# Kernel tuning notes

Hardware: AMD Instinct MI355X
Metric: run time of the kernel (lower is better)

Reference implementation:

```python
import jax, jax.numpy as jnp
import numpy as np

N = 8192
PT_DIM = 3
ENC_DIM = 384
RADIUS = 0.12
ALPHA = 6.0
SQRT_D = ENC_DIM ** 0.5


def setup_inputs() -> dict:
    key = jax.random.key(0)
    k1, k2 = jax.random.split(key)
    pts = jax.random.uniform(k1, (N, PT_DIM), dtype=jnp.float32)  # points in unit cube
    # A corresponds to the (frozen) random-feature matrix: stacked standard normals * alpha
    A = jax.random.normal(k2, (PT_DIM, ENC_DIM), dtype=jnp.float32) * ALPHA
    return {"pts": pts, "A": A}


def reference(pts, A):
    # Radius-ball adjacency: J[i,j] = 1 if ||pts[i]-pts[j]|| < r (dist^2 < r^2, dist >= 0)
    d2 = jnp.sum((pts[:, None, :] - pts[None, :, :]) ** 2, axis=-1)  # (N, N)
    J = (d2 < RADIUS * RADIUS).astype(pts.dtype)                      # (N, N)

    pA = (pts / RADIUS) @ A            # (N, ENC_DIM)
    c, s = jnp.cos(pA), jnp.sin(pA)    # epA = [cos(pA), sin(pA)]

    # Neighbor aggregation: G = J @ epA, done per real/imag part
    Gr = J @ c                          # (N, ENC_DIM)
    Gi = J @ s

    # Complex phase division: (Gr + i Gi) / (cos + i sin)
    G = jax.lax.complex(Gr, Gi) / jax.lax.complex(c, s)

    # Row-wise normalization to norm sqrt(enc_dim)
    G = G / jnp.linalg.norm(G, axis=-1, keepdims=True) * SQRT_D
    return G
```

## Files before the change

### kernel.cpp

```cpp
#include <hip/hip_runtime.h>
#include <hip/hip_fp16.h>
#include <math.h>

#define N_PTS   8192
#define ENC     384
#define NTHREAD 384
#define MAXNB   512
#define NCELL1  8
#define NCELLS  512
#define RADIUS  0.12f

__device__ __forceinline__ void fast_sincos(float x, float& s, float& c) {
    float rev = x * 0.15915494309189535f;
    rev -= rintf(rev);
    s = __builtin_amdgcn_sinf(rev);
    c = __builtin_amdgcn_cosf(rev);
}

__device__ __forceinline__ int cell_of(float x) {
    int c = (int)(x * 8.0f);
    return min(NCELL1 - 1, max(0, c));
}

static const size_t OFF_START_I  = 0;
static const size_t OFF_CURSOR_I = 520;
static const size_t OFF_CELLID_I = 1032;
static const size_t OFF_ORIG_I   = 9224;
static const size_t INT_REGION_B = 17416u * 4;
static const size_t OFF_SPTS_B   = INT_REGION_B;
static const size_t OFF_CS_B     = OFF_SPTS_B + 131072;
static const size_t WS_FULL_B    = OFF_CS_B + (size_t)(N_PTS + 1) * ENC * 2 * 2;
static const size_t WS_SMALL_B   = OFF_CS_B;

__global__ __launch_bounds__(1024) void k_count_scan(const float* __restrict__ pts,
                                                     int* __restrict__ cell_id,
                                                     int* __restrict__ cell_start,
                                                     int* __restrict__ cursor) {
    __shared__ int cnt[NCELLS];
    __shared__ int sc[NCELLS];
    const int t = threadIdx.x;
    if (t < NCELLS) cnt[t] = 0;
    __syncthreads();
    for (int i = t; i < N_PTS; i += 1024) {
        int cx = cell_of(pts[3 * i + 0]);
        int cy = cell_of(pts[3 * i + 1]);
        int cz = cell_of(pts[3 * i + 2]);
        int c = (cx * NCELL1 + cy) * NCELL1 + cz;
        cell_id[i] = c;
        atomicAdd(&cnt[c], 1);
    }
    __syncthreads();
    if (t < NCELLS) sc[t] = cnt[t];
    __syncthreads();
    for (int off = 1; off < NCELLS; off <<= 1) {
        int v = 0;
        if (t < NCELLS && t >= off) v = sc[t - off];
        __syncthreads();
        if (t < NCELLS) sc[t] += v;
        __syncthreads();
    }
    if (t < NCELLS) {
        int excl = sc[t] - cnt[t];
        cell_start[t] = excl;
        cursor[t] = excl;
    }
    if (t == 0) cell_start[NCELLS] = N_PTS;
}

__global__ __launch_bounds__(256) void k_scatter(const float* __restrict__ pts,
                                                 const int* __restrict__ cell_id,
                                                 int* __restrict__ cursor,
                                                 int* __restrict__ orig,
                                                 float4* __restrict__ spts) {
    int i = blockIdx.x * 256 + threadIdx.x;
    if (i >= N_PTS) return;
    int c = cell_id[i];
    int pos = atomicAdd(&cursor[c], 1);
    orig[pos] = i;
    spts[pos] = make_float4(pts[3 * i + 0], pts[3 * i + 1], pts[3 * i + 2], 0.f);
}

__global__ __launch_bounds__(NTHREAD) void k_encode(const float4* __restrict__ spts,
                                                    const float* __restrict__ A,
                                                    __half2* __restrict__ cs) {
    const int p = blockIdx.x;
    const int t = threadIdx.x;
    if (p == N_PTS) {
        cs[(size_t)p * ENC + t] = __floats2half2_rn(0.f, 0.f);
        return;
    }
    float4 P = spts[p];
    float qx = __fdiv_rn(P.x, RADIUS);
    float qy = __fdiv_rn(P.y, RADIUS);
    float qz = __fdiv_rn(P.z, RADIUS);
    float a0 = A[t], a1 = A[ENC + t], a2 = A[2 * ENC + t];
    float pa = fmaf(qz, a2, fmaf(qy, a1, qx * a0));
    float s, c;
    fast_sincos(pa, s, c);
    cs[(size_t)p * ENC + t] = __floats2half2_rn(c, s);
}

__global__ __launch_bounds__(NTHREAD) void k_main(const float4* __restrict__ spts,
                                                  const int* __restrict__ orig,
                                                  const int* __restrict__ cell_start,
                                                  const uint4* __restrict__ cs4,
                                                  const float* __restrict__ A,
                                                  float* __restrict__ out, int out_mode) {
    const int p = (blockIdx.x % 8) * (N_PTS / 8) + blockIdx.x / 8;
    const int t = threadIdx.x, lane = t & 63, wid = t >> 6;

    __shared__ unsigned short nb_idx[MAXNB];
    __shared__ int   nb_cnt;
    __shared__ float comb_a[96][8];
    __shared__ float comb_b[96][8];
    __shared__ float red2[96];
    __shared__ float red_tot;
    if (t == 0) nb_cnt = 0;
    __syncthreads();

    const float4 Pi = spts[p];
    const float xi = Pi.x, yi = Pi.y, zi = Pi.z;
    const double dxi = (double)xi, dyi = (double)yi, dzi = (double)zi;
    const double R2 = (double)0.12 * (double)0.12;
    const float R2_LO = 0.0144f - 1e-6f;
    const float R2_HI = 0.0144f + 1e-6f;

    const int cx = cell_of(xi), cy = cell_of(yi), cz = cell_of(zi);
    const int zlo = max(cz - 1, 0), zhi = min(cz + 1, NCELL1 - 1);

    for (int r = wid; r < 9; r += NTHREAD / 64) {
        int cxx = cx + (r / 3) - 1;
        int cyy = cy + (r % 3) - 1;
        if (cxx < 0 || cxx >= NCELL1 || cyy < 0 || cyy >= NCELL1) continue;
        int base_c = (cxx * NCELL1 + cyy) * NCELL1;
        int lo = cell_start[base_c + zlo];
        int hi = cell_start[base_c + zhi + 1];
        for (int jb = lo; jb < hi; jb += 64) {
            int j = jb + lane;
            bool isnb = false;
            if (j < hi) {
                float4 Pj = spts[j];
                float fdx = Pj.x - xi, fdy = Pj.y - yi, fdz = Pj.z - zi;
                float d2f = fmaf(fdx, fdx, fmaf(fdy, fdy, fdz * fdz));
                if (d2f < R2_LO) {
                    isnb = true;
                } else if (d2f <= R2_HI) {
                    double ddx = (double)Pj.x - dxi, ddy = (double)Pj.y - dyi, ddz = (double)Pj.z - dzi;
                    isnb = (ddx * ddx + ddy * ddy + ddz * ddz) < R2;
                }
            }
            unsigned long long mask = __ballot(isnb);
            if (mask) {
                int leader = __ffsll((long long)mask) - 1;
                int basep = 0;
                if (lane == leader) basep = atomicAdd(&nb_cnt, __popcll(mask));
                basep = __shfl(basep, leader);
                if (isnb) {
                    int pos = basep + __popcll(mask & ((1ull << lane) - 1ull));
                    if (pos < MAXNB) nb_idx[pos] = (unsigned short)j;
                }
            }
        }
    }
    __syncthreads();
    const int nn = min(nb_cnt, MAXNB);
    if (t < 4) {
        int idx = nn + t;
        if (idx < MAXNB) nb_idx[idx] = (unsigned short)N_PTS;
    }
    __syncthreads();
    const int nn_pad = (nn + 3) & ~3;

    const int g = t / 96, q = t - g * 96;
    float4 accR = make_float4(0.f, 0.f, 0.f, 0.f);
    float4 accI = make_float4(0.f, 0.f, 0.f, 0.f);

    #pragma unroll 4
    for (int m = 0; m < nn_pad; m += 4) {
        int j = min((int)nb_idx[m + g], N_PTS);
        uint4 u = cs4[j * 96 + q];
        float2 f0 = __half22float2(*reinterpret_cast<__half2*>(&u.x));
        float2 f1 = __half22float2(*reinterpret_cast<__half2*>(&u.y));
        float2 f2 = __half22float2(*reinterpret_cast<__half2*>(&u.z));
        float2 f3 = __half22float2(*reinterpret_cast<__half2*>(&u.w));
        accR.x += f0.x; accI.x += f0.y;
        accR.y += f1.x; accI.y += f1.y;
        accR.z += f2.x; accI.z += f2.y;
        accR.w += f3.x; accI.w += f3.y;
    }

    if (g == 1) {
        float* d = comb_a[q];
        d[0]=accR.x; d[1]=accR.y; d[2]=accR.z; d[3]=accR.w;
        d[4]=accI.x; d[5]=accI.y; d[6]=accI.z; d[7]=accI.w;
    } else if (g == 3) {
        float* d = comb_b[q];
        d[0]=accR.x; d[1]=accR.y; d[2]=accR.z; d[3]=accR.w;
        d[4]=accI.x; d[5]=accI.y; d[6]=accI.z; d[7]=accI.w;
    }
    __syncthreads();
    if (g == 0) {
        const float* s = comb_a[q];
        accR.x+=s[0]; accR.y+=s[1]; accR.z+=s[2]; accR.w+=s[3];
        accI.x+=s[4]; accI.y+=s[5]; accI.z+=s[6]; accI.w+=s[7];
    } else if (g == 2) {
        const float* s = comb_b[q];
        accR.x+=s[0]; accR.y+=s[1]; accR.z+=s[2]; accR.w+=s[3];
        accI.x+=s[4]; accI.y+=s[5]; accI.z+=s[6]; accI.w+=s[7];
    }
    __syncthreads();
    if (g == 2) {
        float* d = comb_a[q];
        d[0]=accR.x; d[1]=accR.y; d[2]=accR.z; d[3]=accR.w;
        d[4]=accI.x; d[5]=accI.y; d[6]=accI.z; d[7]=accI.w;
    }
    __syncthreads();
    if (g == 0) {
        const float* s = comb_a[q];
        accR.x+=s[0]; accR.y+=s[1]; accR.z+=s[2]; accR.w+=s[3];
        accI.x+=s[4]; accI.y+=s[5]; accI.z+=s[6]; accI.w+=s[7];
    }

    if (g == 0) {
        float m2 = accR.x*accR.x + accI.x*accI.x + accR.y*accR.y + accI.y*accI.y
                 + accR.z*accR.z + accI.z*accI.z + accR.w*accR.w + accI.w*accI.w;
        red2[q] = m2;
    }
    __syncthreads();
    if (t < 64) {
        float v = red2[t] + (t < 32 ? red2[64 + t] : 0.f);
        #pragma unroll
        for (int off = 32; off > 0; off >>= 1) v += __shfl_down(v, off);
        if (t == 0) red_tot = v;
    }
    __syncthreads();

    if (g == 0) {
        const float scale = sqrtf(384.0f / red_tot);
        const float qx = __fdiv_rn(xi, RADIUS);
        const float qy = __fdiv_rn(yi, RADIUS);
        const float qz = __fdiv_rn(zi, RADIUS);
        const int d0 = 4 * q;
        float re[4], im[4];
        #pragma unroll
        for (int k = 0; k < 4; ++k) {
            int d = d0 + k;
            float pa = fmaf(qz, A[2 * ENC + d], fmaf(qy, A[ENC + d], qx * A[d]));
            float sv, cv;
            fast_sincos(pa, sv, cv);
            float gr = (k==0)?accR.x:(k==1)?accR.y:(k==2)?accR.z:accR.w;
            float gi = (k==0)?accI.x:(k==1)?accI.y:(k==2)?accI.z:accI.w;
            re[k] = (gr * cv + gi * sv) * scale;
            im[k] = (gi * cv - gr * sv) * scale;
        }
        const int o = orig[p];
        if (out_mode == 0) {
            ((float4*)out)[o * 96 + q] = make_float4(re[0], re[1], re[2], re[3]);
        } else {
            ((float4*)out)[o * 192 + 2 * q + 0] = make_float4(re[0], im[0], re[1], im[1]);
            ((float4*)out)[o * 192 + 2 * q + 1] = make_float4(re[2], im[2], re[3], im[3]);
        }
    }
}

__global__ __launch_bounds__(NTHREAD) void vecKM_allpairs(const float* __restrict__ pts,
                                                          const float* __restrict__ A,
                                                          float* __restrict__ out, int out_mode) {
    const int i = blockIdx.x;
    const int t = threadIdx.x;
    __shared__ float nb_x[MAXNB], nb_y[MAXNB], nb_z[MAXNB];
    __shared__ int nb_cnt;
    __shared__ float red[8];
    if (t == 0) nb_cnt = 0;
    __syncthreads();
    const float xi = pts[3 * i + 0], yi = pts[3 * i + 1], zi = pts[3 * i + 2];
    const double dxi = xi, dyi = yi, dzi = zi;
    const double R2 = (double)0.12 * (double)0.12;
    const float R2_LO = 0.0144f - 1e-6f, R2_HI = 0.0144f + 1e-6f;
    const int lane = t & 63;
    for (int jb = 0; jb < N_PTS; jb += NTHREAD) {
        const int j = jb + t;
        bool isnb = false;
        float xj = 0.f, yj = 0.f, zj = 0.f;
        if (j < N_PTS) {
            xj = pts[3 * j + 0]; yj = pts[3 * j + 1]; zj = pts[3 * j + 2];
            float fdx = xj - xi, fdy = yj - yi, fdz = zj - zi;
            float d2f = fmaf(fdx, fdx, fmaf(fdy, fdy, fdz * fdz));
            if (d2f < R2_LO) isnb = true;
            else if (d2f <= R2_HI) {
                double dx = (double)xj - dxi, dy = (double)yj - dyi, dz = (double)zj - dzi;
                isnb = (dx * dx + dy * dy + dz * dz) < R2;
            }
        }
        unsigned long long mask = __ballot(isnb);
        if (mask) {
            int leader = __ffsll((long long)mask) - 1;
            int basep = 0;
            if (lane == leader) basep = atomicAdd(&nb_cnt, __popcll(mask));
            basep = __shfl(basep, leader);
            if (isnb) {
                int pos = basep + __popcll(mask & ((1ull << lane) - 1ull));
                if (pos < MAXNB) {
                    nb_x[pos] = (xj - xi) * (1.0f / 0.12f);
                    nb_y[pos] = (yj - yi) * (1.0f / 0.12f);
                    nb_z[pos] = (zj - zi) * (1.0f / 0.12f);
                }
            }
        }
    }
    __syncthreads();
    const int nn = min(nb_cnt, MAXNB);
    const float a0 = A[t], a1 = A[ENC + t], a2 = A[2 * ENC + t];
    float gr = 0.f, gi = 0.f;
    #pragma unroll 4
    for (int m = 0; m < nn; ++m) {
        float pa = fmaf(nb_z[m], a2, fmaf(nb_y[m], a1, nb_x[m] * a0));
        float sv, cv;
        fast_sincos(pa, sv, cv);
        gr += cv; gi += sv;
    }
    float m2 = fmaf(gr, gr, gi * gi);
    #pragma unroll
    for (int off = 32; off > 0; off >>= 1) m2 += __shfl_down(m2, off);
    const int wid = t >> 6;
    if (lane == 0) red[wid] = m2;
    __syncthreads();
    if (t == 0) {
        float tot = 0.f;
        for (int w = 0; w < NTHREAD / 64; ++w) tot += red[w];
        red[7] = tot;
    }
    __syncthreads();
    const float scale = sqrtf(384.0f / red[7]);
    const float re = gr * scale, im = gi * scale;
    if (out_mode == 0) out[i * ENC + t] = re;
    else ((float2*)out)[i * ENC + t] = make_float2(re, im);
}

extern "C" void kernel_launch(void* const* d_in, const int* in_sizes, int n_in,
                              void* d_out, int out_size, void* d_ws, size_t ws_size,
                              hipStream_t stream) {
    const float* pts = (const float*)d_in[0];
    const float* A   = (const float*)d_in[1];
    float* out = (float*)d_out;
    const int out_mode = (out_size >= 2 * N_PTS * ENC) ? 1 : 0;

    if (ws_size >= WS_FULL_B) {
        int*    wsi        = (int*)d_ws;
        int*    cell_start = wsi + OFF_START_I;
        int*    cursor     = wsi + OFF_CURSOR_I;
        int*    cell_id    = wsi + OFF_CELLID_I;
        int*    orig       = wsi + OFF_ORIG_I;
        float4* spts       = (float4*)((char*)d_ws + OFF_SPTS_B);
        __half2* cs        = (__half2*)((char*)d_ws + OFF_CS_B);

        k_count_scan<<<1, 1024, 0, stream>>>(pts, cell_id, cell_start, cursor);
        k_scatter<<<(N_PTS + 255) / 256, 256, 0, stream>>>(pts, cell_id, cursor, orig, spts);
        k_encode<<<N_PTS + 1, NTHREAD, 0, stream>>>(spts, A, cs);
        k_main<<<N_PTS, NTHREAD, 0, stream>>>(spts, orig, cell_start,
                                              (const uint4*)cs, A, out, out_mode);
    } else {
        vecKM_allpairs<<<N_PTS, NTHREAD, 0, stream>>>(pts, A, out, out_mode);
    }
}
```

Measured before the change: 77.50 us.

## Accumulate neighbor sums in packed half2 and batch eight gathers per iteration

Neighbor indices are now stored interleaved per thread group, so each group reads eight indices with a single 16-byte shared load. It then issues eight independent cs gathers per iteration. Accumulation switches from fp32 to packed half2 adds, which drops the per-element half-to-float conversions. This raises memory-level parallelism and cuts ALU work. The cost is fp16 accumulation error over up to hundreds of neighbors, which may break tolerance, and more padding work.

```diff
diff --git a/kernel.cpp b/kernel.cpp
--- a/kernel.cpp
+++ b/kernel.cpp
@@ -30,7 +30,6 @@
 static const size_t OFF_SPTS_B   = INT_REGION_B;
 static const size_t OFF_CS_B     = OFF_SPTS_B + 131072;
 static const size_t WS_FULL_B    = OFF_CS_B + (size_t)(N_PTS + 1) * ENC * 2 * 2;
-static const size_t WS_SMALL_B   = OFF_CS_B;
 
 __global__ __launch_bounds__(1024) void k_count_scan(const float* __restrict__ pts,
                                                      int* __restrict__ cell_id,
@@ -109,7 +108,7 @@
     const int p = (blockIdx.x % 8) * (N_PTS / 8) + blockIdx.x / 8;
     const int t = threadIdx.x, lane = t & 63, wid = t >> 6;
 
-    __shared__ unsigned short nb_idx[MAXNB];
+    __shared__ __align__(16) unsigned short nb_idx_g[4][MAXNB / 4];
     __shared__ int   nb_cnt;
     __shared__ float comb_a[96][8];
     __shared__ float comb_b[96][8];
@@ -157,37 +156,58 @@
                 basep = __shfl(basep, leader);
                 if (isnb) {
                     int pos = basep + __popcll(mask & ((1ull << lane) - 1ull));
-                    if (pos < MAXNB) nb_idx[pos] = (unsigned short)j;
+                    if (pos < MAXNB) nb_idx_g[pos & 3][pos >> 2] = (unsigned short)j;
                 }
             }
         }
     }
     __syncthreads();
     const int nn = min(nb_cnt, MAXNB);
-    if (t < 4) {
-        int idx = nn + t;
-        if (idx < MAXNB) nb_idx[idx] = (unsigned short)N_PTS;
-    }
-    __syncthreads();
-    const int nn_pad = (nn + 3) & ~3;
+    const int P8 = ((((nn + 3) >> 2) + 7) & ~7);
+    {
+        int npad = 4 * P8 - nn;
+        if (t < npad) {
+            int s = nn + t;
+            nb_idx_g[s & 3][s >> 2] = (unsigned short)N_PTS;
+        }
+    }
+    __syncthreads();
 
     const int g = t / 96, q = t - g * 96;
-    float4 accR = make_float4(0.f, 0.f, 0.f, 0.f);
-    float4 accI = make_float4(0.f, 0.f, 0.f, 0.f);
-
-    #pragma unroll 4
-    for (int m = 0; m < nn_pad; m += 4) {
-        int j = min((int)nb_idx[m + g], N_PTS);
-        uint4 u = cs4[j * 96 + q];
-        float2 f0 = __half22float2(*reinterpret_cast<__half2*>(&u.x));
-        float2 f1 = __half22float2(*reinterpret_cast<__half2*>(&u.y));
-        float2 f2 = __half22float2(*reinterpret_cast<__half2*>(&u.z));
-        float2 f3 = __half22float2(*reinterpret_cast<__half2*>(&u.w));
-        accR.x += f0.x; accI.x += f0.y;
-        accR.y += f1.x; accI.y += f1.y;
-        accR.z += f2.x; accI.z += f2.y;
-        accR.w += f3.x; accI.w += f3.y;
-    }
+    const uint4* cs_q = cs4 + q;
+
+    __half2 ac0 = __float2half2_rn(0.f);
+    __half2 ac1 = ac0, ac2 = ac0, ac3 = ac0;
+
+    for (int mb = 0; mb < P8; mb += 8) {
+        uint4 iv = *reinterpret_cast<const uint4*>(&nb_idx_g[g][mb]);
+        int j0 = (int)(iv.x & 0xFFFFu), j1 = (int)(iv.x >> 16);
+        int j2 = (int)(iv.y & 0xFFFFu), j3 = (int)(iv.y >> 16);
+        int j4 = (int)(iv.z & 0xFFFFu), j5 = (int)(iv.z >> 16);
+        int j6 = (int)(iv.w & 0xFFFFu), j7 = (int)(iv.w >> 16);
+        uint4 u0 = cs_q[min(j0, N_PTS) * 96];
+        uint4 u1 = cs_q[min(j1, N_PTS) * 96];
+        uint4 u2 = cs_q[min(j2, N_PTS) * 96];
+        uint4 u3 = cs_q[min(j3, N_PTS) * 96];
+        uint4 u4 = cs_q[min(j4, N_PTS) * 96];
+        uint4 u5 = cs_q[min(j5, N_PTS) * 96];
+        uint4 u6 = cs_q[min(j6, N_PTS) * 96];
+        uint4 u7 = cs_q[min(j7, N_PTS) * 96];
+        #define ACC(U) \
+            ac0 = __hadd2(ac0, *reinterpret_cast<const __half2*>(&U.x)); \
+            ac1 = __hadd2(ac1, *reinterpret_cast<const __half2*>(&U.y)); \
+            ac2 = __hadd2(ac2, *reinterpret_cast<const __half2*>(&U.z)); \
+            ac3 = __hadd2(ac3, *reinterpret_cast<const __half2*>(&U.w));
+        ACC(u0) ACC(u1) ACC(u2) ACC(u3) ACC(u4) ACC(u5) ACC(u6) ACC(u7)
+        #undef ACC
+    }
+
+    float2 f0 = __half22float2(ac0);
+    float2 f1 = __half22float2(ac1);
+    float2 f2 = __half22float2(ac2);
+    float2 f3 = __half22float2(ac3);
+    float4 accR = make_float4(f0.x, f1.x, f2.x, f3.x);
+    float4 accI = make_float4(f0.y, f1.y, f2.y, f3.y);
 
     if (g == 1) {
         float* d = comb_a[q];
```

New measurement: 74.37 us. -4.0%, faster.
